# Optimization experiments

Measured on AMD Instinct MI355X. Metric: run time of the kernel, lower is better.

## Reference

```python
import jax, jax.numpy as jnp
import numpy as np
import hashlib

# Model hyperparameters (from VictorASIFractalLightModel defaults)
B, L, D = 2, 2048, 1024
VOCAB, TOOL_VOCAB = 65536, 128
STEPS = 8            # FractalEmbedding steps -> 2*STEPS = 16 features
N_CONV, N_ATTN = 10, 6
HEADS, Q_GROUPS = 8, 2
HPG = HEADS // Q_GROUPS
HEAD_DIM = D // HEADS
KSIZE = 5
EPS = 1e-5


def _token_to_c(token_ids_np):
    # sha256-based complex constant per token id (exactly as in FractalEmbedding)
    flat = token_ids_np.reshape(-1)
    out = np.empty((flat.size, 2), dtype=np.float32)
    for i, tid in enumerate(flat):
        h = hashlib.sha256(str(int(tid)).encode()).hexdigest()
        out[i, 0] = (int(h[:16], 16) / 2**64 - 0.5) * 2.0
        out[i, 1] = (int(h[16:32], 16) / 2**64 - 0.5) * 2.0
    return out.reshape(token_ids_np.shape + (2,))


def _julia_feats(cs):
    # Vectorized julia iteration, z starts at 0.  cs: [B, L, 2] -> feats [B, L, 2*STEPS]
    cr, ci = cs[..., 0], cs[..., 1]
    zr = jnp.zeros_like(cr)
    zi = jnp.zeros_like(ci)
    feats = []
    for _ in range(STEPS):
        zr, zi = zr * zr - zi * zi + cr, 2.0 * zr * zi + ci
        feats.append(zr)
        feats.append(zi)
    return jnp.stack(feats, axis=-1)


def _layer_norm(x, s, b):
    mu = jnp.mean(x, axis=-1, keepdims=True)
    var = jnp.mean(jnp.square(x - mu), axis=-1, keepdims=True)
    return (x - mu) * jax.lax.rsqrt(var + EPS) * s + b


def _conv_block(x, dw_w, dw_b, pw_w, pw_b, ln_s, ln_b):
    # x: [B, L, D] -> depthwise conv (k=5, same pad) -> pointwise conv to 2D -> GLU -> residual LN
    xc = jnp.transpose(x, (0, 2, 1))  # [B, D, L]
    y = jax.lax.conv_general_dilated(xc, dw_w, (1,), [(KSIZE // 2, KSIZE // 2)],
                                     dimension_numbers=("NCH", "OIH", "NCH"),
                                     feature_group_count=D) + dw_b[None, :, None]
    y = jax.lax.conv_general_dilated(y, pw_w, (1,), [(0, 0)],
                                     dimension_numbers=("NCH", "OIH", "NCH")) + pw_b[None, :, None]
    y = jnp.transpose(y, (0, 2, 1))  # [B, L, 2D]
    a, gate = jnp.split(y, 2, axis=-1)
    return _layer_norm(x + a * jax.nn.sigmoid(gate), ln_s, ln_b)


def _attention(x, qw, kvw, ow, ln_s, ln_b):
    # Grouped-query attention with an explicit (unfused) score tensor, per the source.
    Bx, Lx, Dx = x.shape
    q = (x @ qw).reshape(Bx, Lx, Q_GROUPS, HPG, HEAD_DIM)
    kv = (x @ kvw).reshape(Bx, Lx, HEADS, 2, HEAD_DIM)
    k = kv[..., 0, :].reshape(Bx, Lx, Q_GROUPS, HPG, HEAD_DIM)
    v = kv[..., 1, :].reshape(Bx, Lx, Q_GROUPS, HPG, HEAD_DIM)
    scale = HEAD_DIM ** -0.5
    scores = jnp.einsum("bqghd,bkghd->bghqk", q, k) * scale  # [B, g, hpg, Lq, Lk]
    attn = jax.nn.softmax(scores, axis=-1)
    out = jnp.einsum("bghqk,bkghd->bqghd", attn, v).reshape(Bx, Lx, Dx)
    return _layer_norm(x + out @ ow, ln_s, ln_b)


def setup_inputs() -> dict:
    key = jax.random.key(0)
    ks = jax.random.split(key, 10)
    token_ids = jax.random.randint(ks[0], (B, L), 0, VOCAB)
    cs = jnp.asarray(_token_to_c(np.asarray(token_ids)))
    return {
        "token_ids": token_ids,
        "cs": cs,
        "proj_w": jax.random.normal(ks[1], (2 * STEPS, D), dtype=jnp.float32) * 0.25,
        "emb_scale": jnp.ones((1,), dtype=jnp.float32),
        "conv_dw_w": jax.random.normal(ks[2], (N_CONV, D, 1, KSIZE), dtype=jnp.float32) * 0.2,
        "conv_dw_b": jnp.zeros((N_CONV, D), dtype=jnp.float32),
        "conv_pw_w": jax.random.normal(ks[3], (N_CONV, 2 * D, D, 1), dtype=jnp.float32) * (D ** -0.5),
        "conv_pw_b": jnp.zeros((N_CONV, 2 * D), dtype=jnp.float32),
        "conv_ln_s": jnp.ones((N_CONV, D), dtype=jnp.float32),
        "conv_ln_b": jnp.zeros((N_CONV, D), dtype=jnp.float32),
        "attn_q_w": jax.random.normal(ks[4], (N_ATTN, D, D), dtype=jnp.float32) * (D ** -0.5),
        "attn_kv_w": jax.random.normal(ks[5], (N_ATTN, D, 2 * D), dtype=jnp.float32) * (D ** -0.5),
        "attn_out_w": jax.random.normal(ks[6], (N_ATTN, D, D), dtype=jnp.float32) * (D ** -0.5),
        "attn_ln_s": jnp.ones((N_ATTN, D), dtype=jnp.float32),
        "attn_ln_b": jnp.zeros((N_ATTN, D), dtype=jnp.float32),
        "lm_w": jax.random.normal(ks[7], (D, VOCAB), dtype=jnp.float32) * (D ** -0.5),
        "tool_w": jax.random.normal(ks[8], (D, TOOL_VOCAB), dtype=jnp.float32) * (D ** -0.5),
        "tool_b": jnp.zeros((TOOL_VOCAB,), dtype=jnp.float32),
    }


def reference(token_ids, cs, proj_w, emb_scale, conv_dw_w, conv_dw_b, conv_pw_w, conv_pw_b,
              conv_ln_s, conv_ln_b, attn_q_w, attn_kv_w, attn_out_w, attn_ln_s, attn_ln_b,
              lm_w, tool_w, tool_b):
    feats = _julia_feats(cs)                 # [B, L, 16]
    h = (feats @ proj_w) * emb_scale         # FractalEmbedding
    for i in range(N_CONV):
        h = _conv_block(h, conv_dw_w[i], conv_dw_b[i], conv_pw_w[i], conv_pw_b[i],
                        conv_ln_s[i], conv_ln_b[i])
    for i in range(N_ATTN):
        h = _attention(h, attn_q_w[i], attn_kv_w[i], attn_out_w[i], attn_ln_s[i], attn_ln_b[i])
    # ReplayMemoryStack is a side-effecting identity on h.
    last = h[:, -1, :]
    gen_logits = last @ lm_w
    tool_logits = last @ tool_w + tool_b
    return gen_logits, tool_logits
```

## Files before the change

### kernel.cpp

```cpp
#include <hip/hip_runtime.h>
#include <hip/hip_bf16.h>
#include <math.h>

#define B_ 2
#define L_ 2048
#define D_ 1024
#define VOCAB_ 65536
#define TOOLV_ 128
#define NCONV_ 10
#define NATTN_ 6
#define HEADS_ 8
#define HD_ 128
#define EPS_ 1e-5f

typedef short bf16x8 __attribute__((ext_vector_type(8)));
typedef short short4v __attribute__((ext_vector_type(4)));
typedef float f32x4 __attribute__((ext_vector_type(4)));
#define MFMA16(a,b,c) __builtin_amdgcn_mfma_f32_16x16x32_bf16(a, b, c, 0, 0, 0)

__device__ inline short f2bf(float f) {
  __hip_bfloat16 h = __float2bfloat16(f);
  return *reinterpret_cast<short*>(&h);
}

__device__ __forceinline__ void gld16(const void* g, void* l) {
  __builtin_amdgcn_global_load_lds(
      (const __attribute__((address_space(1))) unsigned int*)g,
      (__attribute__((address_space(3))) unsigned int*)l, 16, 0, 0);
}

__device__ __forceinline__ void sync_prefetch() {
  asm volatile("s_waitcnt vmcnt(0)" ::: "memory");
  __builtin_amdgcn_s_barrier();
  __builtin_amdgcn_sched_barrier(0);
}

__global__ __launch_bounds__(256) void julia_proj_k(const float* __restrict__ cs,
    const float* __restrict__ pw, const float* __restrict__ esc, float* __restrict__ h) {
  int row = blockIdx.x;
  float cr = cs[2*(size_t)row], ci = cs[2*(size_t)row+1];
  float f[16];
  float zr = 0.f, zi = 0.f;
  #pragma unroll
  for (int s = 0; s < 8; ++s) {
    float nzr = zr*zr - zi*zi + cr;
    float nzi = 2.f*zr*zi + ci;
    zr = nzr; zi = nzi;
    f[2*s] = zr; f[2*s+1] = zi;
  }
  float e = esc[0];
  int d = threadIdx.x * 4;
  float4 acc = {0.f, 0.f, 0.f, 0.f};
  #pragma unroll
  for (int i = 0; i < 16; ++i) {
    float4 pv = *(const float4*)(pw + i*D_ + d);
    acc.x += f[i]*pv.x; acc.y += f[i]*pv.y; acc.z += f[i]*pv.z; acc.w += f[i]*pv.w;
  }
  acc.x *= e; acc.y *= e; acc.z *= e; acc.w *= e;
  *(float4*)(h + (size_t)row*D_ + d) = acc;
}

__global__ __launch_bounds__(256) void dwconv_k(const float* __restrict__ x,
    const float* __restrict__ w, const float* __restrict__ bias, short* __restrict__ y) {
  int idx = blockIdx.x*256 + threadIdx.x;
  int d = (idx & (D_/4 - 1)) * 4;
  int bl = idx >> 8;
  int l = bl & (L_-1);
  size_t bbase = (size_t)(bl >> 11) * L_;
  float4 acc = *(const float4*)(bias + d);
  float wr[4][5];
  #pragma unroll
  for (int j = 0; j < 4; ++j)
    #pragma unroll
    for (int k = 0; k < 5; ++k) wr[j][k] = w[(d+j)*5 + k];
  #pragma unroll
  for (int k = 0; k < 5; ++k) {
    int ll = l + k - 2;
    if (ll >= 0 && ll < L_) {
      float4 xv = *(const float4*)(x + (bbase + ll)*D_ + d);
      acc.x += xv.x*wr[0][k]; acc.y += xv.y*wr[1][k];
      acc.z += xv.z*wr[2][k]; acc.w += xv.w*wr[3][k];
    }
  }
  short4v o = { f2bf(acc.x), f2bf(acc.y), f2bf(acc.z), f2bf(acc.w) };
  ((short4v*)y)[idx] = o;
}

__global__ __launch_bounds__(256) void ln_dwconv_k(const float* __restrict__ hIn,
    const float* __restrict__ glu, const float* __restrict__ lns,
    const float* __restrict__ lnb, const float* __restrict__ dww,
    const float* __restrict__ dwb, float* __restrict__ hOut,
    short* __restrict__ abf) {
  __shared__ float lds[12][1028];
  const int tid = threadIdx.x;
  const int wv = tid >> 6, ln = tid & 63;
  const int r0 = blockIdx.x * 8;
  const int bb = r0 >> 11;

  float4 sv[4], bv[4];
  #pragma unroll
  for (int q = 0; q < 4; ++q) {
    int d = ln*4 + q*256;
    sv[q] = *(const float4*)(lns + d);
    bv[q] = *(const float4*)(lnb + d);
  }

  #pragma unroll
  for (int i = 0; i < 3; ++i) {
    int lr = wv*3 + i;
    int gl = r0 - 2 + lr;
    bool valid = (gl >= (bb << 11)) && (gl < ((bb + 1) << 11));
    if (valid) {
      float4 v4[4];
      float ssum = 0.f;
      #pragma unroll
      for (int q = 0; q < 4; ++q) {
        int d = ln*4 + q*256;
        float4 xv = *(const float4*)(hIn + (size_t)gl*D_ + d);
        float4 pv = *(const float4*)(glu + (size_t)gl*D_ + d);
        v4[q].x = xv.x+pv.x; v4[q].y = xv.y+pv.y;
        v4[q].z = xv.z+pv.z; v4[q].w = xv.w+pv.w;
        ssum += v4[q].x + v4[q].y + v4[q].z + v4[q].w;
      }
      #pragma unroll
      for (int mask = 1; mask < 64; mask <<= 1) ssum += __shfl_xor(ssum, mask);
      float mu = ssum * (1.f/D_);
      float vs = 0.f;
      #pragma unroll
      for (int q = 0; q < 4; ++q) {
        float dx = v4[q].x-mu, dy = v4[q].y-mu, dz = v4[q].z-mu, dw = v4[q].w-mu;
        vs += dx*dx + dy*dy + dz*dz + dw*dw;
      }
      #pragma unroll
      for (int mask = 1; mask < 64; mask <<= 1) vs += __shfl_xor(vs, mask);
      float rr = 1.f/sqrtf(vs*(1.f/D_) + EPS_);
      #pragma unroll
      for (int q = 0; q < 4; ++q) {
        int d = ln*4 + q*256;
        float4 o4;
        o4.x = (v4[q].x-mu)*rr*sv[q].x + bv[q].x;
        o4.y = (v4[q].y-mu)*rr*sv[q].y + bv[q].y;
        o4.z = (v4[q].z-mu)*rr*sv[q].z + bv[q].z;
        o4.w = (v4[q].w-mu)*rr*sv[q].w + bv[q].w;
        *(float4*)&lds[lr][d] = o4;
        if (lr >= 2 && lr < 10)
          *(float4*)(hOut + (size_t)gl*D_ + d) = o4;
      }
    } else {
      float4 z = {0.f,0.f,0.f,0.f};
      #pragma unroll
      for (int q = 0; q < 4; ++q)
        *(float4*)&lds[lr][ln*4 + q*256] = z;
    }
  }
  __syncthreads();

  int o = tid >> 5;
  int cb = (tid & 31) * 4;
  int grow = r0 + o;
  #pragma unroll
  for (int p = 0; p < 8; ++p) {
    int d = cb + p*128;
    float wf[20];
    #pragma unroll
    for (int j = 0; j < 5; ++j)
      *(float4*)&wf[j*4] = *(const float4*)(dww + d*5 + j*4);
    float4 acc = *(const float4*)(dwb + d);
    #pragma unroll
    for (int k = 0; k < 5; ++k) {
      float4 lv = *(const float4*)&lds[o + k][d];
      acc.x += lv.x * wf[k];
      acc.y += lv.y * wf[5 + k];
      acc.z += lv.z * wf[10 + k];
      acc.w += lv.w * wf[15 + k];
    }
    short4v ov = { f2bf(acc.x), f2bf(acc.y), f2bf(acc.z), f2bf(acc.w) };
    *(short4v*)(abf + (size_t)grow*D_ + d) = ov;
  }
}

__global__ __launch_bounds__(256) void cvt_perm_k(const float* __restrict__ W,
    short* __restrict__ out) {
  int z = blockIdx.y;
  int i4 = blockIdx.x*256 + threadIdx.x;
  int e = i4*4;
  int r = e >> 10, k = e & 1023;
  int t = r >> 7, wn = (r >> 6) & 1, j = r & 63;
  int u = t*64 + wn*32 + (j & 31);
  int src = (j < 32) ? u : 1024 + u;
  const float* p = W + ((size_t)z*2048 + src)*1024 + k;
  float4 v = *(const float4*)p;
  short4v s = { f2bf(v.x), f2bf(v.y), f2bf(v.z), f2bf(v.w) };
  *(short4v*)(out + ((size_t)z*2048 + r)*1024 + k) = s;
}

__global__ __launch_bounds__(256) void transp_bf16_k(const float* __restrict__ W0,
    short* __restrict__ WT0, int K, int N, size_t srcStride, size_t dstStride) {
  const float* W = W0 + blockIdx.z*srcStride;
  short* WT = WT0 + blockIdx.z*dstStride;
  __shared__ short t[32][33];
  int n0 = blockIdx.x*32, k0 = blockIdx.y*32;
  int tx = threadIdx.x & 31, ty = threadIdx.x >> 5;
  #pragma unroll
  for (int i = 0; i < 4; ++i) {
    int k = ty + i*8;
    t[tx][k] = f2bf(W[(size_t)(k0+k)*N + n0 + tx]);
  }
  __syncthreads();
  #pragma unroll
  for (int i = 0; i < 4; ++i) {
    int n = ty + i*8;
    WT[(size_t)(n0+n)*K + k0 + tx] = t[n][tx];
  }
}

__global__ __launch_bounds__(256) void transp_qo_k(const float* __restrict__ Wq,
    const float* __restrict__ Wo, short* __restrict__ WTq, short* __restrict__ WTo) {
  int z = blockIdx.z;
  const float* W;
  short* WT;
  if (z < NATTN_) { W = Wq + (size_t)z*D_*D_; WT = WTq + (size_t)z*3*D_*D_; }
  else { W = Wo + (size_t)(z-NATTN_)*D_*D_; WT = WTo + (size_t)(z-NATTN_)*D_*D_; }
  __shared__ short t[32][33];
  int n0 = blockIdx.x*32, k0 = blockIdx.y*32;
  int tx = threadIdx.x & 31, ty = threadIdx.x >> 5;
  #pragma unroll
  for (int i = 0; i < 4; ++i) {
    int k = ty + i*8;
    t[tx][k] = f2bf(W[(size_t)(k0+k)*D_ + n0 + tx]);
  }
  __syncthreads();
  #pragma unroll
  for (int i = 0; i < 4; ++i) {
    int n = ty + i*8;
    WT[(size_t)(n0+n)*D_ + k0 + tx] = t[n][tx];
  }
}

template<int MODE, int BN>
__global__ __launch_bounds__(256) void gemm_bf16(const short* __restrict__ A,
    const short* __restrict__ Bt, const float* __restrict__ bias,
    float* __restrict__ C, short* __restrict__ obf,
    short* __restrict__ kbf, short* __restrict__ vtbf,
    float scale, int M, int N, int K) {
  constexpr int NI = BN/32;
  __shared__ short As[2][128*32];
  __shared__ short Bs[2][BN*32];
  const int tid  = threadIdx.x;
  const int lane = tid & 63;
  const int wave = tid >> 6;
  const int wm = wave >> 1, wn = wave & 1;
  const int g = lane >> 4, c = lane & 15;

  int flat = blockIdx.y * gridDim.x + blockIdx.x;
  int nwg  = gridDim.x * gridDim.y;
  int swz  = (flat & 7) * (nwg >> 3) + (flat >> 3);
  const int m0 = (swz & 31) * 128;
  const int n0 = (swz >> 5) * BN;

  f32x4 acc[4][NI];
  #pragma unroll
  for (int i = 0; i < 4; ++i)
    #pragma unroll
    for (int j = 0; j < NI; ++j) acc[i][j] = (f32x4){0.f,0.f,0.f,0.f};

  const int srow = wave*16 + (lane>>2);
  const int scol = (lane&3)*8;
  const short* aSrc0 = A + (size_t)(m0 + srow)*K + scol;
  const short* aSrc1 = aSrc0 + (size_t)64*K;
  const short* bSrc0 = Bt + (size_t)(n0 + srow)*K + scol;
  const short* bSrc1 = bSrc0 + (size_t)64*K;
  const int woff = wave*512;

  gld16(aSrc0, &As[0][woff]);
  gld16(aSrc1, &As[0][woff + 2048]);
  gld16(bSrc0, &Bs[0][woff]);
  if (BN == 128) gld16(bSrc1, &Bs[0][woff + 2048]);
  sync_prefetch();

  const int nt = K >> 5;
  int cur = 0;
  for (int t = 0; t < nt; ++t) {
    if (t + 1 < nt) {
      int k0 = (t + 1) << 5;
      gld16(aSrc0 + k0, &As[cur^1][woff]);
      gld16(aSrc1 + k0, &As[cur^1][woff + 2048]);
      gld16(bSrc0 + k0, &Bs[cur^1][woff]);
      if (BN == 128) gld16(bSrc1 + k0, &Bs[cur^1][woff + 2048]);
    }
    bf16x8 af[4], bfr[NI];
    #pragma unroll
    for (int mi = 0; mi < 4; ++mi)
      af[mi] = *(const bf16x8*)&As[cur][(wm*64 + mi*16 + c)*32 + g*8];
    #pragma unroll
    for (int ni = 0; ni < NI; ++ni)
      bfr[ni] = *(const bf16x8*)&Bs[cur][(wn*(BN/2) + ni*16 + c)*32 + g*8];
    #pragma unroll
    for (int mi = 0; mi < 4; ++mi)
      #pragma unroll
      for (int ni = 0; ni < NI; ++ni)
        acc[mi][ni] = MFMA16(af[mi], bfr[ni], acc[mi][ni]);
    if (t + 1 < nt) {
      sync_prefetch();
      cur ^= 1;
    }
  }

  if (MODE == 4) {
    #pragma unroll
    for (int mi = 0; mi < 4; ++mi) {
      int row = m0 + wm*64 + mi*16 + g*4;
      #pragma unroll
      for (int ni = 0; ni < 2; ++ni) {
        int u = (n0 >> 7)*64 + wn*32 + ni*16 + c;
        float ba = bias[u], bg = bias[1024 + u];
        #pragma unroll
        for (int r = 0; r < 4; ++r) {
          float a  = acc[mi][ni][r]   + ba;
          float gt = acc[mi][ni+2][r] + bg;
          C[(size_t)(row+r)*1024 + u] = a / (1.f + expf(-gt));
        }
      }
    }
    return;
  }

  #pragma unroll
  for (int mi = 0; mi < 4; ++mi) {
    int row = m0 + wm*64 + mi*16 + g*4;
    #pragma unroll
    for (int ni = 0; ni < NI; ++ni) {
      int col = n0 + wn*(BN/2) + ni*16 + c;
      if (MODE == 0) {
        #pragma unroll
        for (int r = 0; r < 4; ++r)
          C[(size_t)(row+r)*N + col] = acc[mi][ni][r];
      } else {
        if (col < 1024) {
          #pragma unroll
          for (int r = 0; r < 4; ++r)
            obf[(size_t)(row+r)*1024 + col] = f2bf(acc[mi][ni][r]*scale);
        } else {
          int col2 = col - 1024;
          int hh = col2 >> 8, jj = (col2 >> 7) & 1, d = col2 & 127;
          int bb = row >> 11, l = row & 2047;
          size_t bh = (size_t)bb*8 + hh;
          if (jj == 0) {
            #pragma unroll
            for (int r = 0; r < 4; ++r)
              kbf[(bh*L_ + l + r)*128 + d] = f2bf(acc[mi][ni][r]);
          } else {
            #pragma unroll
            for (int r = 0; r < 4; ++r)
              vtbf[(bh*128 + d)*L_ + l + r] = f2bf(acc[mi][ni][r]);
          }
        }
      }
    }
  }
}

__global__ __launch_bounds__(256) void resid_ln_k(float* __restrict__ h,
    const float* __restrict__ proj, const float* __restrict__ s, const float* __restrict__ b,
    short* __restrict__ bo) {
  int row = blockIdx.x;
  int tid = threadIdx.x;
  int d = tid*4;
  float* xr = h + (size_t)row*D_;
  const float* pr = proj + (size_t)row*D_;
  __shared__ float red[256];
  float4 xv = *(const float4*)(xr + d);
  float4 pv = *(const float4*)(pr + d);
  float v[4] = { xv.x+pv.x, xv.y+pv.y, xv.z+pv.z, xv.w+pv.w };
  red[tid] = v[0]+v[1]+v[2]+v[3]; __syncthreads();
  for (int st = 128; st > 0; st >>= 1) { if (tid < st) red[tid] += red[tid+st]; __syncthreads(); }
  float mu = red[0] * (1.f/D_); __syncthreads();
  float lv = 0.f;
  #pragma unroll
  for (int j = 0; j < 4; ++j) { float dd = v[j]-mu; lv += dd*dd; }
  red[tid] = lv; __syncthreads();
  for (int st = 128; st > 0; st >>= 1) { if (tid < st) red[tid] += red[tid+st]; __syncthreads(); }
  float var = red[0] * (1.f/D_);
  float r = 1.f/sqrtf(var + EPS_);
  float4 sv = *(const float4*)(s + d);
  float4 bv = *(const float4*)(b + d);
  float4 o;
  o.x = (v[0]-mu)*r*sv.x + bv.x;
  o.y = (v[1]-mu)*r*sv.y + bv.y;
  o.z = (v[2]-mu)*r*sv.z + bv.z;
  o.w = (v[3]-mu)*r*sv.w + bv.w;
  *(float4*)(xr + d) = o;
  if (bo) {
    short4v ob = { f2bf(o.x), f2bf(o.y), f2bf(o.z), f2bf(o.w) };
    *(short4v*)(bo + (size_t)row*D_ + d) = ob;
  }
}

#define PPITCH 72
__global__ __launch_bounds__(256) void attn2_k(const short* __restrict__ qbf,
    const short* __restrict__ kbf, const short* __restrict__ vtbf,
    short* __restrict__ obf) {
  __shared__ short Ks[2][64*128];
  __shared__ short Vts[2][128*64];
  __shared__ short Ps[4*16*PPITCH];

  const int tid  = threadIdx.x;
  const int wave = tid >> 6;
  const int lane = tid & 63;
  const int g    = lane >> 4;
  const int c    = lane & 15;

  int flat = blockIdx.x;
  int swz  = (flat & 7)*64 + (flat >> 3);
  const int qt = swz & 31;
  const int hh = (swz >> 5) & 7;
  const int b  = swz >> 8;
  const int q0 = qt*64 + wave*16;
  const size_t bh = (size_t)(b*HEADS_ + hh);

  bf16x8 qf[4];
  {
    const short* Qp = qbf + ((size_t)(b*L_ + q0 + c))*D_ + hh*HD_;
    #pragma unroll
    for (int kd = 0; kd < 4; ++kd)
      qf[kd] = *(const bf16x8*)(Qp + kd*32 + g*8);
  }

  f32x4 O[8];
  #pragma unroll
  for (int i = 0; i < 8; ++i) O[i] = (f32x4){0.f,0.f,0.f,0.f};
  float mrun[4] = {-INFINITY,-INFINITY,-INFINITY,-INFINITY};
  float lrun[4] = {0.f,0.f,0.f,0.f};
  short* Pw = Ps + wave*16*PPITCH;

  const short* kBase = kbf + bh*L_*128;
  const short* vBase = vtbf + bh*128*L_;

  auto stage = [&](int t, int buf) {
    #pragma unroll
    for (int rd = 0; rd < 4; ++rd) {
      int slot = rd*256 + tid;
      int kr = slot >> 4, kj = slot & 15;
      int vr = slot >> 3, vj = slot & 7;
      gld16(kBase + ((size_t)(t*64 + kr))*128 + ((kj ^ (kr & 15)) * 8),
            (char*)&Ks[buf][0] + (rd*256 + wave*64)*16);
      gld16(vBase + (size_t)vr*L_ + t*64 + ((vj ^ (vr & 7)) * 8),
            (char*)&Vts[buf][0] + (rd*256 + wave*64)*16);
    }
  };

  stage(0, 0);
  sync_prefetch();
  int cur = 0;
  const int NT = L_/64;

  for (int t = 0; t < NT; ++t) {
    if (t + 1 < NT) stage(t + 1, cur^1);

    f32x4 s[4];
    #pragma unroll
    for (int nc = 0; nc < 4; ++nc) {
      s[nc] = (f32x4){0.f,0.f,0.f,0.f};
      int R = nc*16 + c;
      #pragma unroll
      for (int kd = 0; kd < 4; ++kd) {
        bf16x8 kf = *(const bf16x8*)&Ks[cur][R*128 + (((kd*4 + g) ^ (R & 15)) * 8)];
        s[nc] = MFMA16(qf[kd], kf, s[nc]);
      }
    }

    float tm[4], rsum[4], alpha[4];
    #pragma unroll
    for (int r = 0; r < 4; ++r)
      tm[r] = fmaxf(fmaxf(s[0][r], s[1][r]), fmaxf(s[2][r], s[3][r]));
    #pragma unroll
    for (int r = 0; r < 4; ++r) {
      #pragma unroll
      for (int mask = 1; mask <= 8; mask <<= 1)
        tm[r] = fmaxf(tm[r], __shfl_xor(tm[r], mask));
      float mnew = fmaxf(mrun[r], tm[r]);
      alpha[r] = expf(mrun[r] - mnew);
      mrun[r] = mnew;
      rsum[r] = 0.f;
    }
    #pragma unroll
    for (int nc = 0; nc < 4; ++nc)
      #pragma unroll
      for (int r = 0; r < 4; ++r) {
        float p = expf(s[nc][r] - mrun[r]);
        s[nc][r] = p;
        rsum[r] += p;
      }
    #pragma unroll
    for (int r = 0; r < 4; ++r) {
      #pragma unroll
      for (int mask = 1; mask <= 8; mask <<= 1)
        rsum[r] += __shfl_xor(rsum[r], mask);
      lrun[r] = lrun[r]*alpha[r] + rsum[r];
    }
    #pragma unroll
    for (int nc = 0; nc < 8; ++nc)
      #pragma unroll
      for (int r = 0; r < 4; ++r) O[nc][r] *= alpha[r];

    #pragma unroll
    for (int nc = 0; nc < 4; ++nc)
      #pragma unroll
      for (int r = 0; r < 4; ++r)
        Pw[(g*4+r)*PPITCH + nc*16 + c] = f2bf(s[nc][r]);
    asm volatile("s_waitcnt lgkmcnt(0)" ::: "memory");
    bf16x8 pa0 = *(const bf16x8*)&Pw[c*PPITCH + g*8];
    bf16x8 pa1 = *(const bf16x8*)&Pw[c*PPITCH + 32 + g*8];

    #pragma unroll
    for (int ks = 0; ks < 2; ++ks) {
      #pragma unroll
      for (int nc = 0; nc < 8; ++nc) {
        int R = nc*16 + c;
        bf16x8 vf = *(const bf16x8*)&Vts[cur][R*64 + (((ks*4 + g) ^ (R & 7)) * 8)];
        O[nc] = MFMA16(ks ? pa1 : pa0, vf, O[nc]);
      }
    }

    if (t + 1 < NT) {
      sync_prefetch();
      cur ^= 1;
    }
  }

  short* ob = obf + ((size_t)(b*L_ + q0))*D_ + hh*HD_;
  #pragma unroll
  for (int r = 0; r < 4; ++r) {
    float inv = 1.f / lrun[r];
    #pragma unroll
    for (int nc = 0; nc < 8; ++nc)
      ob[(size_t)(g*4+r)*D_ + nc*16 + c] = f2bf(O[nc][r] * inv);
  }
}

__global__ __launch_bounds__(256) void lm_head_part_k(const float* __restrict__ h,
    const float* __restrict__ lm_w, float* __restrict__ part) {
  int tid = threadIdx.x;
  int n = (blockIdx.x*256 + tid)*4;
  int ks = blockIdx.y;
  __shared__ float last0[128], last1[128];
  const float* h0 = h + ((size_t)0*L_ + (L_-1))*D_ + ks*128;
  const float* h1 = h + ((size_t)1*L_ + (L_-1))*D_ + ks*128;
  if (tid < 128) { last0[tid] = h0[tid]; last1[tid] = h1[tid]; }
  __syncthreads();
  float4 a0 = {0.f,0.f,0.f,0.f}, a1 = {0.f,0.f,0.f,0.f};
  const float* wp = lm_w + (size_t)(ks*128)*VOCAB_ + n;
  for (int kk = 0; kk < 128; ++kk) {
    float4 wv = *(const float4*)(wp + (size_t)kk*VOCAB_);
    float c0 = last0[kk], c1 = last1[kk];
    a0.x += c0*wv.x; a0.y += c0*wv.y; a0.z += c0*wv.z; a0.w += c0*wv.w;
    a1.x += c1*wv.x; a1.y += c1*wv.y; a1.z += c1*wv.z; a1.w += c1*wv.w;
  }
  *(float4*)(part + ((size_t)ks*2 + 0)*VOCAB_ + n) = a0;
  *(float4*)(part + ((size_t)ks*2 + 1)*VOCAB_ + n) = a1;
}

__global__ __launch_bounds__(256) void lm_head_red_k(const float* __restrict__ part,
    float* __restrict__ out) {
  int i = blockIdx.x*256 + threadIdx.x;
  int j = (i*4) / VOCAB_;
  int n = (i*4) & (VOCAB_-1);
  float4 acc = {0.f,0.f,0.f,0.f};
  #pragma unroll
  for (int ks = 0; ks < 8; ++ks) {
    float4 v = *(const float4*)(part + ((size_t)ks*2 + j)*VOCAB_ + n);
    acc.x += v.x; acc.y += v.y; acc.z += v.z; acc.w += v.w;
  }
  *(float4*)(out + (size_t)j*VOCAB_ + n) = acc;
}

__global__ __launch_bounds__(128) void tool_head_k(const float* __restrict__ h,
    const float* __restrict__ tw, const float* __restrict__ tb, float* __restrict__ out) {
  int b = blockIdx.x;
  int tid = threadIdx.x;
  __shared__ float last[D_];
  const float* hr = h + ((size_t)b*L_ + (L_-1))*D_;
  for (int d = tid; d < D_; d += 128) last[d] = hr[d];
  __syncthreads();
  float acc = tb[tid];
  for (int k = 0; k < D_; ++k) acc += last[k]*tw[(size_t)k*TOOLV_ + tid];
  out[(size_t)2*VOCAB_ + (size_t)b*TOOLV_ + tid] = acc;
}

extern "C" void kernel_launch(void* const* d_in, const int* in_sizes, int n_in,
                              void* d_out, int out_size, void* d_ws, size_t ws_size,
                              hipStream_t stream) {
  const float* cs        = (const float*)d_in[1];
  const float* proj_w    = (const float*)d_in[2];
  const float* emb_scale = (const float*)d_in[3];
  const float* conv_dw_w = (const float*)d_in[4];
  const float* conv_dw_b = (const float*)d_in[5];
  const float* conv_pw_w = (const float*)d_in[6];
  const float* conv_pw_b = (const float*)d_in[7];
  const float* conv_ln_s = (const float*)d_in[8];
  const float* conv_ln_b = (const float*)d_in[9];
  const float* attn_q_w  = (const float*)d_in[10];
  const float* attn_kv_w = (const float*)d_in[11];
  const float* attn_out_w= (const float*)d_in[12];
  const float* attn_ln_s = (const float*)d_in[13];
  const float* attn_ln_b = (const float*)d_in[14];
  const float* lm_w      = (const float*)d_in[15];
  const float* tool_w    = (const float*)d_in[16];
  const float* tool_b    = (const float*)d_in[17];

  const int M = B_*L_;
  float* hA   = (float*)d_ws;
  float* hB   = hA   + (size_t)M*D_;
  float* buf2 = hB   + (size_t)M*D_;
  short* kbf  = (short*)(buf2 + (size_t)M*2*D_);
  short* vtbf = kbf + (size_t)B_*HEADS_*L_*128;
  short* abf  = (short*)(vtbf + (size_t)B_*HEADS_*128*L_);
  short* wconv= abf + (size_t)M*D_;
  short* wqkv = wconv + (size_t)NCONV_*2*D_*D_;
  short* wout = wqkv + (size_t)NATTN_*3*D_*D_;
  float* lmpart = (float*)(wout + (size_t)NATTN_*D_*D_);
  short* qbf  = (short*)(buf2 + (size_t)M*D_);

  const float scale = 0.088388347648318447f;

  {
    cvt_perm_k<<<dim3((2*D_*D_/4)/256, NCONV_), 256, 0, stream>>>(conv_pw_w, wconv);
    transp_qo_k<<<dim3(D_/32, D_/32, 2*NATTN_), 256, 0, stream>>>(
        attn_q_w, attn_out_w, wqkv, wout);
    transp_bf16_k<<<dim3((2*D_)/32, D_/32, NATTN_), 256, 0, stream>>>(
        attn_kv_w, wqkv + (size_t)D_*D_, D_, 2*D_, (size_t)D_*2*D_, (size_t)3*D_*D_);
  }

  julia_proj_k<<<M, 256, 0, stream>>>(cs, proj_w, emb_scale, hA);

  dwconv_k<<<(M*D_/4)/256, 256, 0, stream>>>(hA, conv_dw_w, conv_dw_b, abf);

  float* hc = hA;
  float* hn = hB;
  for (int i = 0; i < NCONV_ - 1; ++i) {
    gemm_bf16<4, 128><<<dim3(M/128, (2*D_)/128), 256, 0, stream>>>(
        abf, wconv + (size_t)i*2*D_*D_, conv_pw_b + (size_t)i*2*D_,
        buf2, nullptr, nullptr, nullptr, 1.f, M, 2*D_, D_);
    ln_dwconv_k<<<M/8, 256, 0, stream>>>(hc, buf2,
        conv_ln_s + (size_t)i*D_, conv_ln_b + (size_t)i*D_,
        conv_dw_w + (size_t)(i+1)*D_*5, conv_dw_b + (size_t)(i+1)*D_,
        hn, abf);
    float* tmp = hc; hc = hn; hn = tmp;
  }
  gemm_bf16<4, 128><<<dim3(M/128, (2*D_)/128), 256, 0, stream>>>(
      abf, wconv + (size_t)(NCONV_-1)*2*D_*D_, conv_pw_b + (size_t)(NCONV_-1)*2*D_,
      buf2, nullptr, nullptr, nullptr, 1.f, M, 2*D_, D_);
  resid_ln_k<<<M, 256, 0, stream>>>(hc, buf2,
      conv_ln_s + (size_t)(NCONV_-1)*D_, conv_ln_b + (size_t)(NCONV_-1)*D_, abf);

  for (int i = 0; i < NATTN_; ++i) {
    gemm_bf16<3, 128><<<dim3(M/128, (3*D_)/128), 256, 0, stream>>>(
        abf, wqkv + (size_t)i*3*D_*D_, nullptr, nullptr, qbf, kbf, vtbf,
        scale, M, 3*D_, D_);
    attn2_k<<<(L_/64)*HEADS_*B_, 256, 0, stream>>>(qbf, kbf, vtbf, abf);
    gemm_bf16<0, 64><<<dim3(M/128, D_/64), 256, 0, stream>>>(
        abf, wout + (size_t)i*D_*D_, nullptr, buf2, nullptr, nullptr, nullptr,
        1.f, M, D_, D_);
    resid_ln_k<<<M, 256, 0, stream>>>(hc, buf2, attn_ln_s + (size_t)i*D_,
                                      attn_ln_b + (size_t)i*D_,
                                      (i < NATTN_-1) ? abf : (short*)nullptr);
  }

  lm_head_part_k<<<dim3(VOCAB_/1024, 8), 256, 0, stream>>>(hc, lm_w, lmpart);
  lm_head_red_k<<<(2*VOCAB_/4)/256, 256, 0, stream>>>(lmpart, (float*)d_out);
  tool_head_k<<<B_, 128, 0, stream>>>(hc, tool_w, tool_b, (float*)d_out);
}
```

Measured before the change: 1.692 ms.

## Triple-buffer GEMM LDS tiles with partial vmcnt waits

Moves the bf16 GEMM main loop from double to triple buffering in shared memory. Loads now run two K-tiles ahead, and each iteration waits only for the oldest tile (vmcnt of 3 or 4) instead of draining every outstanding load. This is meant to hide global-load latency behind the MFMA work. In exchange the kernel uses more LDS per block, which can lower occupancy, and it relies on hand-written waitcnt counts matching the number of loads issued per stage.

```diff
diff --git a/kernel.cpp b/kernel.cpp
--- a/kernel.cpp
+++ b/kernel.cpp
@@ -244,8 +244,8 @@
     short* __restrict__ kbf, short* __restrict__ vtbf,
     float scale, int M, int N, int K) {
   constexpr int NI = BN/32;
-  __shared__ short As[2][128*32];
-  __shared__ short Bs[2][BN*32];
+  __shared__ short As[3][128*32];
+  __shared__ short Bs[3][BN*32];
   const int tid  = threadIdx.x;
   const int lane = tid & 63;
   const int wave = tid >> 6;
@@ -272,21 +272,27 @@
   const short* bSrc1 = bSrc0 + (size_t)64*K;
   const int woff = wave*512;
 
-  gld16(aSrc0, &As[0][woff]);
-  gld16(aSrc1, &As[0][woff + 2048]);
-  gld16(bSrc0, &Bs[0][woff]);
-  if (BN == 128) gld16(bSrc1, &Bs[0][woff + 2048]);
-  sync_prefetch();
+  auto stage = [&](int t, int b) {
+    int k0 = t << 5;
+    gld16(aSrc0 + k0, &As[b][woff]);
+    gld16(aSrc1 + k0, &As[b][woff + 2048]);
+    gld16(bSrc0 + k0, &Bs[b][woff]);
+    if (BN == 128) gld16(bSrc1 + k0, &Bs[b][woff + 2048]);
+  };
 
   const int nt = K >> 5;
+  stage(0, 0);
+  stage(1, 1);
+  if constexpr (BN == 128) asm volatile("s_waitcnt vmcnt(4)" ::: "memory");
+  else                     asm volatile("s_waitcnt vmcnt(3)" ::: "memory");
+  __builtin_amdgcn_s_barrier();
+  __builtin_amdgcn_sched_barrier(0);
+
   int cur = 0;
   for (int t = 0; t < nt; ++t) {
-    if (t + 1 < nt) {
-      int k0 = (t + 1) << 5;
-      gld16(aSrc0 + k0, &As[cur^1][woff]);
-      gld16(aSrc1 + k0, &As[cur^1][woff + 2048]);
-      gld16(bSrc0 + k0, &Bs[cur^1][woff]);
-      if (BN == 128) gld16(bSrc1 + k0, &Bs[cur^1][woff + 2048]);
+    if (t + 2 < nt) {
+      int b = cur + 2; if (b >= 3) b -= 3;
+      stage(t + 2, b);
     }
     bf16x8 af[4], bfr[NI];
     #pragma unroll
@@ -301,8 +307,15 @@
       for (int ni = 0; ni < NI; ++ni)
         acc[mi][ni] = MFMA16(af[mi], bfr[ni], acc[mi][ni]);
     if (t + 1 < nt) {
-      sync_prefetch();
-      cur ^= 1;
+      if (t + 2 < nt) {
+        if constexpr (BN == 128) asm volatile("s_waitcnt vmcnt(4)" ::: "memory");
+        else                     asm volatile("s_waitcnt vmcnt(3)" ::: "memory");
+      } else {
+        asm volatile("s_waitcnt vmcnt(0)" ::: "memory");
+      }
+      __builtin_amdgcn_s_barrier();
+      __builtin_amdgcn_sched_barrier(0);
+      cur = (cur == 2) ? 0 : cur + 1;
     }
   }
 
```

Result: no change. 1.713 ms (+1.3%).
